# Kernel tuning notes

Hardware: AMD Instinct MI355X
Metric: run time of the kernel (lower is better)

The kernel has to match this reference:

```python
import jax, jax.numpy as jnp
import numpy as np

N_ENT = 50000
N_REL = 200
N_EDGE = 1_000_000
D = 64


def setup_inputs() -> dict:
    key = jax.random.key(0)
    ks = jax.random.split(key, 12)
    src = jax.random.randint(ks[0], (N_EDGE,), 0, N_ENT)
    rel = jax.random.randint(ks[1], (N_EDGE,), 0, N_REL)
    dst = jax.random.randint(ks[2], (N_EDGE,), 0, N_ENT)
    triples = jnp.stack([src, rel, dst], axis=1).astype(jnp.int64)  # [E,3]
    s = 1.0 / np.sqrt(D)
    return {
        "emb_e": jax.random.normal(ks[3], (N_ENT, D), jnp.float32) * s,
        "re_att": jax.random.normal(ks[4], (N_REL,), jnp.float32) * 0.1,
        "W1": jax.random.normal(ks[5], (D, D), jnp.float32) * s,
        "W2": jax.random.normal(ks[6], (D, D), jnp.float32) * s,
        "W3": jax.random.normal(ks[7], (D, D), jnp.float32) * s,
        "u": jax.random.normal(ks[8], (3 * D,), jnp.float32) * s,
        "en_weight": jax.random.normal(ks[9], (D, D), jnp.float32) * s,
        "re_weight": jax.random.normal(ks[10], (D, D), jnp.float32) * s,
        "re_spec": jax.random.normal(ks[11], (D,), jnp.float32) * s,
        "triples": triples,
    }


def _forward(emb_e, re_att, W1, W2, W3, u, en_weight, re_weight, re_spec, triples):
    src = triples[:, 0]
    rel = triples[:, 1]
    dst = triples[:, 2]
    n = emb_e.shape[0]

    def wgc(x, W):
        # relation-weighted message passing: out[s] += w[r] * x[d]
        msg = jax.ops.segment_sum(x[dst] * re_att[rel][:, None], src, num_segments=n)
        return jnp.tanh((x + msg) @ W)

    x = wgc(emb_e, W1)
    x = wgc(x, W2)
    x = wgc(x, W3)

    # GAT-style edge scores: e = LeakyReLU(u . [W_en h_i ; W_re r_spec ; W_en h_j])
    d = x.shape[1]
    hs = x @ en_weight.T                       # [N,d] = (en_weight @ h)^T rows
    z_src = hs @ u[:d]                         # [N]
    z_dst = hs @ u[2 * d:]                     # [N]
    z_mid = u[d:2 * d] @ (re_weight @ re_spec)  # scalar, same for every edge
    scores = jax.nn.leaky_relu(z_src[src] + z_mid + z_dst[dst], 0.01)  # [E]

    # softmax normalized over ALL triples (global denominator, per source code)
    alpha = jax.nn.softmax(scores)

    # out[src] += alpha_e * x[dst]
    out = jax.ops.segment_sum(alpha[:, None] * x[dst], src, num_segments=n)
    return out


def reference(emb_e, re_att, W1, W2, W3, u, en_weight, re_weight, re_spec, triples):
    return _forward(emb_e, re_att, W1, W2, W3, u, en_weight, re_weight, re_spec, triples)
```

## Files before the change

### kernel.cpp

```cpp
#include <hip/hip_runtime.h>
#include <math.h>

#define N_ENT  50000
#define N_REL  200
#define N_EDGE 1000000
#define CHUNK  196
#define ECH    7813
#define NRNG   6250

#define WS_MISC   0
#define WS_ZSUM   128
#define WS_ZMID   192
#define WS_AV     256
#define WS_BV     512
#define WS_BSUM   0x000E0000
#define WS_BBASE  0x000F0000
#define WS_CNT8   0x00100000
#define WS_RBASE  0x00300000
#define WS_TOT    0x00500000
#define WS_OFFS   0x00540000
#define WS_ZSRC   0x00580000
#define WS_ZDST   0x005C0000
#define WS_SNODE  0x00600000
#define WS_EPK    0x00640000
#define WS_EA     0x00A40000
#define WS_EB     0x00E40000
#define WS_XB1    0x00A40000
#define WS_XB0    0x01240000

__device__ __forceinline__ float bflo(unsigned u) { return __uint_as_float(u << 16); }
__device__ __forceinline__ float bfhi(unsigned u) { return __uint_as_float(u & 0xffff0000u); }
__device__ __forceinline__ unsigned short f2bf(float f) {
  unsigned u = __float_as_uint(f);
  unsigned r = ((u >> 16) & 1u) + 0x7fffu;
  return (unsigned short)((u + r) >> 16);
}
__device__ __forceinline__ float lanebc(float v, int k) {
  return __uint_as_float((unsigned)__builtin_amdgcn_readlane((int)__float_as_uint(v), k));
}
__device__ __forceinline__ float fast_tanh(float x) {
  float ex = __expf(2.f * x);
  return 1.f - __fdividef(2.f, ex + 1.f);
}
__device__ __forceinline__ void fma8(float* acc, float wt, uint4 q) {
  acc[0] += wt * bflo(q.x); acc[1] += wt * bfhi(q.x);
  acc[2] += wt * bflo(q.y); acc[3] += wt * bfhi(q.y);
  acc[4] += wt * bflo(q.z); acc[5] += wt * bfhi(q.z);
  acc[6] += wt * bflo(q.w); acc[7] += wt * bfhi(q.w);
}

__global__ void k_init(const void* tri, int* cnt8, int* misc, double* zsum) {
  int i = blockIdx.x * blockDim.x + threadIdx.x;
  if (i < 8 * N_ENT) cnt8[i] = 0;
  if (blockIdx.x == 0 && threadIdx.x < 64) {
    int l = threadIdx.x;
    int z = ((const int*)tri)[2 * l + 1];
    unsigned long long m = __ballot(z == 0);
    if (l == 0) { misc[0] = (m == ~0ull) ? 1 : 0; *zsum = 0.0; }
  }
}

__global__ void k_conv(const float* __restrict__ x, unsigned short* __restrict__ xb) {
  int i = blockIdx.x * blockDim.x + threadIdx.x;
  if (i >= N_ENT * 16) return;
  float4 v = ((const float4*)x)[i];
  ushort4 o;
  o.x = f2bf(v.x); o.y = f2bf(v.y); o.z = f2bf(v.z); o.w = f2bf(v.w);
  ((ushort4*)xb)[i] = o;
}

__global__ void k_decode(const void* tri, int* __restrict__ cnt8,
                         unsigned* __restrict__ ea, unsigned* __restrict__ eb,
                         const int* misc) {
  int is64 = misc[0];
  int rep = blockIdx.x & 7;
  int stride = gridDim.x * blockDim.x;
  if (is64) {
    const long long* t = (const long long*)tri;
    for (int e = blockIdx.x * blockDim.x + threadIdx.x; e < N_EDGE; e += stride) {
      int s = (int)t[3 * e], r = (int)t[3 * e + 1], d = (int)t[3 * e + 2];
      int rk = atomicAdd(&cnt8[rep * N_ENT + s], 1);
      ea[e] = ((unsigned)s << 16) | ((unsigned)rep << 13) | (unsigned)rk;
      eb[e] = ((unsigned)r << 16) | (unsigned)d;
    }
  } else {
    const int* t = (const int*)tri;
    for (int e = blockIdx.x * blockDim.x + threadIdx.x; e < N_EDGE; e += stride) {
      int s = t[3 * e], r = t[3 * e + 1], d = t[3 * e + 2];
      int rk = atomicAdd(&cnt8[rep * N_ENT + s], 1);
      ea[e] = ((unsigned)s << 16) | ((unsigned)rep << 13) | (unsigned)rk;
      eb[e] = ((unsigned)r << 16) | (unsigned)d;
    }
  }
}

__global__ void k_merge(const int* __restrict__ cnt8, int* __restrict__ rbase,
                        int* __restrict__ tot) {
  int s = blockIdx.x * blockDim.x + threadIdx.x;
  if (s >= N_ENT) return;
  int run = 0;
#pragma unroll
  for (int rep = 0; rep < 8; rep++) {
    rbase[rep * N_ENT + s] = run;
    run += cnt8[rep * N_ENT + s];
  }
  tot[s] = run;
}

__global__ void k_scanA(const int* __restrict__ counts, int* __restrict__ bsum) {
  __shared__ int sm[4];
  int t = threadIdx.x;
  int i = blockIdx.x * CHUNK + t;
  int v = (t < CHUNK && i < N_ENT) ? counts[i] : 0;
  for (int o = 32; o; o >>= 1) v += __shfl_down(v, o);
  if ((t & 63) == 0) sm[t >> 6] = v;
  __syncthreads();
  if (t == 0) bsum[blockIdx.x] = sm[0] + sm[1] + sm[2] + sm[3];
}

__global__ void k_scanB(const int* __restrict__ bsum, int* __restrict__ bbase, int* __restrict__ offs) {
  __shared__ int sm[256];
  int t = threadIdx.x;
  int v = bsum[t];
  sm[t] = v;
  __syncthreads();
  for (int d = 1; d < 256; d <<= 1) {
    int x = (t >= d) ? sm[t - d] : 0;
    __syncthreads();
    sm[t] += x;
    __syncthreads();
  }
  bbase[t] = sm[t] - v;
  if (t == 255) offs[N_ENT] = sm[255];
}

__global__ void k_scanC(const int* __restrict__ counts, const int* __restrict__ bbase,
                        int* __restrict__ offs) {
  __shared__ int sm[256];
  int t = threadIdx.x;
  int i = blockIdx.x * CHUNK + t;
  int v = (t < CHUNK && i < N_ENT) ? counts[i] : 0;
  sm[t] = v;
  __syncthreads();
  for (int d = 1; d < 256; d <<= 1) {
    int x = (t >= d) ? sm[t - d] : 0;
    __syncthreads();
    sm[t] += x;
    __syncthreads();
  }
  if (t < CHUNK && i < N_ENT)
    offs[i] = bbase[blockIdx.x] + sm[t] - v;
}

__global__ void k_scatter(const unsigned* __restrict__ ea, const unsigned* __restrict__ eb,
                          const int* __restrict__ offs, const int* __restrict__ rbase,
                          unsigned* __restrict__ epk) {
  int q = blockIdx.x >> 3, x = blockIdx.x & 7;
  int lo = q * ECH, hi = lo + ECH;
  if (hi > N_EDGE) hi = N_EDGE;
  for (int e = lo + threadIdx.x; e < hi; e += 256) {
    unsigned a = ea[e];
    int s = a >> 16;
    if (s / NRNG == x) {
      int rep = (a >> 13) & 7;
      int rk = a & 8191;
      epk[offs[s] + rbase[rep * N_ENT + s] + rk] = eb[e];
    }
  }
}

__global__ void k_pre(const float* u, const float* enw, const float* rew, const float* rsp,
                      float* a, float* b, float* zmid) {
  int k = threadIdx.x;
  float aa = 0.f, bb = 0.f;
  for (int j = 0; j < 64; j++) {
    float w = enw[j * 64 + k];
    aa += u[j] * w;
    bb += u[128 + j] * w;
  }
  a[k] = aa; b[k] = bb;
  float t = 0.f;
  for (int c = 0; c < 64; c++) t += rew[k * 64 + c] * rsp[c];
  t *= u[64 + k];
  for (int o = 32; o; o >>= 1) t += __shfl_down(t, o);
  if (k == 0) *zmid = t;
}

template <int EPI>
__global__ void __launch_bounds__(256) k_wgc(
    const unsigned short* __restrict__ xb, const float* __restrict__ W,
    const int* __restrict__ offs, const unsigned* __restrict__ epk,
    const float* __restrict__ re_att, unsigned short* __restrict__ yb,
    const float* __restrict__ a, const float* __restrict__ b,
    float* __restrict__ zsrc, float* __restrict__ zdst) {
  __shared__ float s_att[N_REL];
  for (int t = threadIdx.x; t < N_REL; t += 256) s_att[t] = re_att[t];
  __syncthreads();
  int wid = (blockIdx.x * blockDim.x + threadIdx.x) >> 6;
  int lane = threadIdx.x & 63;
  if (wid >= N_ENT) return;
  int node = wid;
  int g = lane >> 3, c8 = (lane & 7) * 8;
  int e0 = offs[node], e1 = offs[node + 1];
  float acc[8] = {0.f, 0.f, 0.f, 0.f, 0.f, 0.f, 0.f, 0.f};
  {
    uint4 q = *(const uint4*)(xb + (size_t)node * 64 + c8);
    fma8(acc, (g == 0) ? 1.f : 0.f, q);
  }
  for (int e = e0; e < e1; e += 16) {
    int ia = e + g, ib = ia + 8;
    bool va = ia < e1, vb = ib < e1;
    unsigned pa = epk[va ? ia : e0];
    unsigned pb = epk[vb ? ib : e0];
    float wa = va ? s_att[pa >> 16] : 0.f;
    float wb = vb ? s_att[pb >> 16] : 0.f;
    uint4 qa = *(const uint4*)(xb + (size_t)(pa & 0xffffu) * 64 + c8);
    uint4 qb = *(const uint4*)(xb + (size_t)(pb & 0xffffu) * 64 + c8);
    fma8(acc, wa, qa);
    fma8(acc, wb, qb);
  }
#pragma unroll
  for (int off = 8; off <= 32; off <<= 1)
#pragma unroll
    for (int c = 0; c < 8; c++) acc[c] += __shfl_xor(acc[c], off);
  float o = 0.f;
#pragma unroll
  for (int j = 0; j < 8; j++)
#pragma unroll
    for (int c = 0; c < 8; c++)
      o += lanebc(acc[c], j) * W[(j * 8 + c) * 64 + lane];
  float yv = fast_tanh(o);
  yb[(size_t)node * 64 + lane] = f2bf(yv);
  if (EPI) {
    float za = yv * a[lane], zb = yv * b[lane];
    for (int s = 32; s; s >>= 1) { za += __shfl_down(za, s); zb += __shfl_down(zb, s); }
    if (lane == 0) { zsrc[node] = za; zdst[node] = zb; }
  }
}

__global__ void __launch_bounds__(256) k_out(
    const unsigned short* __restrict__ xb, const int* __restrict__ offs,
    const unsigned* __restrict__ epk, const float* __restrict__ zs,
    const float* __restrict__ zd, const float* zmid,
    float* __restrict__ out, float* __restrict__ snode) {
  int wid = (blockIdx.x * blockDim.x + threadIdx.x) >> 6;
  int lane = threadIdx.x & 63;
  if (wid >= N_ENT) return;
  int node = wid;
  int g = lane >> 3, c8 = (lane & 7) * 8;
  float zi = zs[node] + *zmid;
  float acc[8] = {0.f, 0.f, 0.f, 0.f, 0.f, 0.f, 0.f, 0.f};
  float s0 = 0.f;
  int e0 = offs[node], e1 = offs[node + 1];
  for (int e = e0; e < e1; e += 16) {
    int ia = e + g, ib = ia + 8;
    bool va = ia < e1, vb = ib < e1;
    unsigned pa = epk[va ? ia : e0];
    unsigned pb = epk[vb ? ib : e0];
    int da = pa & 0xffffu, db = pb & 0xffffu;
    float ca = zi + zd[da];
    float cb = zi + zd[db];
    ca = ca >= 0.f ? ca : 0.01f * ca;
    cb = cb >= 0.f ? cb : 0.01f * cb;
    float wa = va ? __expf(ca) : 0.f;
    float wb = vb ? __expf(cb) : 0.f;
    uint4 qa = *(const uint4*)(xb + (size_t)da * 64 + c8);
    uint4 qb = *(const uint4*)(xb + (size_t)db * 64 + c8);
    fma8(acc, wa, qa);
    fma8(acc, wb, qb);
    s0 += wa + wb;
  }
#pragma unroll
  for (int off = 8; off <= 32; off <<= 1) {
#pragma unroll
    for (int c = 0; c < 8; c++) acc[c] += __shfl_xor(acc[c], off);
    s0 += __shfl_xor(s0, off);
  }
  if (lane < 8) {
    float4* p = (float4*)(out + (size_t)node * 64 + lane * 8);
    p[0] = make_float4(acc[0], acc[1], acc[2], acc[3]);
    p[1] = make_float4(acc[4], acc[5], acc[6], acc[7]);
  }
  if (lane == 0) snode[node] = s0;
}

__global__ void k_red(const float* __restrict__ snode, double* zsum) {
  int stride = gridDim.x * blockDim.x;
  double s = 0.0;
  for (int i = blockIdx.x * blockDim.x + threadIdx.x; i < N_ENT; i += stride)
    s += (double)snode[i];
  for (int o = 32; o; o >>= 1) s += __shfl_down(s, o);
  __shared__ double ws_[4];
  if ((threadIdx.x & 63) == 0) ws_[threadIdx.x >> 6] = s;
  __syncthreads();
  if (threadIdx.x == 0)
    atomicAdd(zsum, ws_[0] + ws_[1] + ws_[2] + ws_[3]);
}

__global__ void k_norm(float* __restrict__ out, const double* zsum) {
  int i = blockIdx.x * blockDim.x + threadIdx.x;
  if (i >= N_ENT * 16) return;
  float invZ = (float)(1.0 / *zsum);
  float4 v = ((float4*)out)[i];
  v.x *= invZ; v.y *= invZ; v.z *= invZ; v.w *= invZ;
  ((float4*)out)[i] = v;
}

extern "C" void kernel_launch(void* const* d_in, const int* in_sizes, int n_in,
                              void* d_out, int out_size, void* d_ws, size_t ws_size,
                              hipStream_t stream) {
  const float* emb   = (const float*)d_in[0];
  const float* reatt = (const float*)d_in[1];
  const float* W1    = (const float*)d_in[2];
  const float* W2    = (const float*)d_in[3];
  const float* W3    = (const float*)d_in[4];
  const float* u     = (const float*)d_in[5];
  const float* enw   = (const float*)d_in[6];
  const float* rew   = (const float*)d_in[7];
  const float* rsp   = (const float*)d_in[8];
  const void*  tri   = d_in[9];

  char* ws = (char*)d_ws;
  int*            misc   = (int*)(ws + WS_MISC);
  double*         zsum   = (double*)(ws + WS_ZSUM);
  float*          zmid   = (float*)(ws + WS_ZMID);
  float*          av     = (float*)(ws + WS_AV);
  float*          bv     = (float*)(ws + WS_BV);
  int*            bsum   = (int*)(ws + WS_BSUM);
  int*            bbase  = (int*)(ws + WS_BBASE);
  int*            cnt8   = (int*)(ws + WS_CNT8);
  int*            rbase  = (int*)(ws + WS_RBASE);
  int*            tot    = (int*)(ws + WS_TOT);
  int*            offs   = (int*)(ws + WS_OFFS);
  float*          zsrc   = (float*)(ws + WS_ZSRC);
  float*          zdst   = (float*)(ws + WS_ZDST);
  float*          snode  = (float*)(ws + WS_SNODE);
  unsigned*       epk    = (unsigned*)(ws + WS_EPK);
  unsigned*       ea     = (unsigned*)(ws + WS_EA);
  unsigned*       eb     = (unsigned*)(ws + WS_EB);
  unsigned short* xb0    = (unsigned short*)(ws + WS_XB0);
  unsigned short* xb1    = (unsigned short*)(ws + WS_XB1);
  float*          out    = (float*)d_out;

  k_init<<<1563, 256, 0, stream>>>(tri, cnt8, misc, zsum);
  k_conv<<<3125, 256, 0, stream>>>(emb, xb0);
  k_decode<<<4096, 256, 0, stream>>>(tri, cnt8, ea, eb, misc);
  k_merge<<<196, 256, 0, stream>>>(cnt8, rbase, tot);
  k_scanA<<<256, 256, 0, stream>>>(tot, bsum);
  k_scanB<<<1, 256, 0, stream>>>(bsum, bbase, offs);
  k_scanC<<<256, 256, 0, stream>>>(tot, bbase, offs);
  k_scatter<<<1024, 256, 0, stream>>>(ea, eb, offs, rbase, epk);
  k_pre<<<1, 64, 0, stream>>>(u, enw, rew, rsp, av, bv, zmid);

  int nb = (N_ENT * 64 + 255) / 256;
  k_wgc<0><<<nb, 256, 0, stream>>>(xb0, W1, offs, epk, reatt, xb1, nullptr, nullptr, nullptr, nullptr);
  k_wgc<0><<<nb, 256, 0, stream>>>(xb1, W2, offs, epk, reatt, xb0, nullptr, nullptr, nullptr, nullptr);
  k_wgc<1><<<nb, 256, 0, stream>>>(xb0, W3, offs, epk, reatt, xb1, av, bv, zsrc, zdst);

  k_out<<<nb, 256, 0, stream>>>(xb1, offs, epk, zsrc, zdst, zmid, out, snode);
  k_red<<<196, 256, 0, stream>>>(snode, zsum);
  k_norm<<<3125, 256, 0, stream>>>(out, zsum);
}
```

Measured before the change: 243.8 us.

## Replace global-atomic CSR build with shared-memory chunked histogram and scatter

Edge bucketing by source no longer uses global atomics into 8 replicated count arrays. It now builds per-chunk histograms in LDS for each of 8 node ranges, scans them per node across 64 chunks to get chunk bases, and scatters using LDS atomics for local ranks. This removes contended global atomics and the large count-array zeroing, at the cost of an extra pass over the source ids and a serial 64-step scan per node. The gather loops also clamp invalid lanes to row 0 instead of reading a stale index.

```diff
diff --git a/kernel.cpp b/kernel.cpp
--- a/kernel.cpp
+++ b/kernel.cpp
@@ -5,7 +5,9 @@
 #define N_REL  200
 #define N_EDGE 1000000
 #define CHUNK  196
-#define ECH    7813
+#define NCH    64
+#define ECH2   15625
+#define NPART  8
 #define NRNG   6250
 
 #define WS_MISC   0
@@ -13,20 +15,19 @@
 #define WS_ZMID   192
 #define WS_AV     256
 #define WS_BV     512
-#define WS_BSUM   0x000E0000
-#define WS_BBASE  0x000F0000
-#define WS_CNT8   0x00100000
-#define WS_RBASE  0x00300000
-#define WS_TOT    0x00500000
-#define WS_OFFS   0x00540000
-#define WS_ZSRC   0x00580000
-#define WS_ZDST   0x005C0000
-#define WS_SNODE  0x00600000
-#define WS_EPK    0x00640000
-#define WS_EA     0x00A40000
-#define WS_EB     0x00E40000
-#define WS_XB1    0x00A40000
-#define WS_XB0    0x01240000
+#define WS_BSUM   0x00010000
+#define WS_BBASE  0x00011000
+#define WS_TOT    0x00040000
+#define WS_OFFS   0x00080000
+#define WS_ZSRC   0x000C0000
+#define WS_ZDST   0x00100000
+#define WS_SNODE  0x00140000
+#define WS_SRCS   0x00180000
+#define WS_EB     0x00380000
+#define WS_EPK    0x00780000
+#define WS_HIST   0x00B80000
+#define WS_XB1    0x00B80000
+#define WS_XB0    0x01200000
 
 __device__ __forceinline__ float bflo(unsigned u) { return __uint_as_float(u << 16); }
 __device__ __forceinline__ float bfhi(unsigned u) { return __uint_as_float(u & 0xffff0000u); }
@@ -49,9 +50,7 @@
   acc[6] += wt * bflo(q.w); acc[7] += wt * bfhi(q.w);
 }
 
-__global__ void k_init(const void* tri, int* cnt8, int* misc, double* zsum) {
-  int i = blockIdx.x * blockDim.x + threadIdx.x;
-  if (i < 8 * N_ENT) cnt8[i] = 0;
+__global__ void k_init(const void* tri, int* misc, double* zsum) {
   if (blockIdx.x == 0 && threadIdx.x < 64) {
     int l = threadIdx.x;
     int z = ((const int*)tri)[2 * l + 1];
@@ -69,40 +68,52 @@
   ((ushort4*)xb)[i] = o;
 }
 
-__global__ void k_decode(const void* tri, int* __restrict__ cnt8,
-                         unsigned* __restrict__ ea, unsigned* __restrict__ eb,
-                         const int* misc) {
+__global__ void k_decode(const void* tri, unsigned short* __restrict__ srcs,
+                         unsigned* __restrict__ eb, const int* misc) {
   int is64 = misc[0];
-  int rep = blockIdx.x & 7;
   int stride = gridDim.x * blockDim.x;
   if (is64) {
     const long long* t = (const long long*)tri;
     for (int e = blockIdx.x * blockDim.x + threadIdx.x; e < N_EDGE; e += stride) {
       int s = (int)t[3 * e], r = (int)t[3 * e + 1], d = (int)t[3 * e + 2];
-      int rk = atomicAdd(&cnt8[rep * N_ENT + s], 1);
-      ea[e] = ((unsigned)s << 16) | ((unsigned)rep << 13) | (unsigned)rk;
+      srcs[e] = (unsigned short)s;
       eb[e] = ((unsigned)r << 16) | (unsigned)d;
     }
   } else {
     const int* t = (const int*)tri;
     for (int e = blockIdx.x * blockDim.x + threadIdx.x; e < N_EDGE; e += stride) {
       int s = t[3 * e], r = t[3 * e + 1], d = t[3 * e + 2];
-      int rk = atomicAdd(&cnt8[rep * N_ENT + s], 1);
-      ea[e] = ((unsigned)s << 16) | ((unsigned)rep << 13) | (unsigned)rk;
+      srcs[e] = (unsigned short)s;
       eb[e] = ((unsigned)r << 16) | (unsigned)d;
     }
   }
 }
 
-__global__ void k_merge(const int* __restrict__ cnt8, int* __restrict__ rbase,
-                        int* __restrict__ tot) {
+__global__ void __launch_bounds__(256) k_hist(const unsigned short* __restrict__ srcs,
+                                              unsigned short* __restrict__ hist) {
+  __shared__ unsigned h[NRNG];
+  int c = blockIdx.x >> 3, x = blockIdx.x & 7;
+  int lo = x * NRNG;
+  for (int i = threadIdx.x; i < NRNG; i += 256) h[i] = 0u;
+  __syncthreads();
+  int e0 = c * ECH2, e1 = e0 + ECH2;
+  for (int e = e0 + threadIdx.x; e < e1; e += 256) {
+    int rel = (int)srcs[e] - lo;
+    if ((unsigned)rel < NRNG) atomicAdd(&h[rel], 1u);
+  }
+  __syncthreads();
+  for (int i = threadIdx.x; i < NRNG; i += 256)
+    hist[c * N_ENT + lo + i] = (unsigned short)h[i];
+}
+
+__global__ void k_scanH(unsigned short* __restrict__ hist, int* __restrict__ tot) {
   int s = blockIdx.x * blockDim.x + threadIdx.x;
   if (s >= N_ENT) return;
   int run = 0;
-#pragma unroll
-  for (int rep = 0; rep < 8; rep++) {
-    rbase[rep * N_ENT + s] = run;
-    run += cnt8[rep * N_ENT + s];
+  for (int c = 0; c < NCH; c++) {
+    int v = hist[c * N_ENT + s];
+    hist[c * N_ENT + s] = (unsigned short)run;
+    run += v;
   }
   tot[s] = run;
 }
@@ -152,19 +163,22 @@
     offs[i] = bbase[blockIdx.x] + sm[t] - v;
 }
 
-__global__ void k_scatter(const unsigned* __restrict__ ea, const unsigned* __restrict__ eb,
-                          const int* __restrict__ offs, const int* __restrict__ rbase,
-                          unsigned* __restrict__ epk) {
-  int q = blockIdx.x >> 3, x = blockIdx.x & 7;
-  int lo = q * ECH, hi = lo + ECH;
-  if (hi > N_EDGE) hi = N_EDGE;
-  for (int e = lo + threadIdx.x; e < hi; e += 256) {
-    unsigned a = ea[e];
-    int s = a >> 16;
-    if (s / NRNG == x) {
-      int rep = (a >> 13) & 7;
-      int rk = a & 8191;
-      epk[offs[s] + rbase[rep * N_ENT + s] + rk] = eb[e];
+__global__ void __launch_bounds__(256) k_scatter(
+    const unsigned short* __restrict__ srcs, const unsigned* __restrict__ eb,
+    const unsigned short* __restrict__ cbase, const int* __restrict__ offs,
+    unsigned* __restrict__ epk) {
+  __shared__ unsigned h[NRNG];
+  int c = blockIdx.x >> 3, x = blockIdx.x & 7;
+  int lo = x * NRNG;
+  for (int i = threadIdx.x; i < NRNG; i += 256) h[i] = 0u;
+  __syncthreads();
+  int e0 = c * ECH2, e1 = e0 + ECH2;
+  for (int e = e0 + threadIdx.x; e < e1; e += 256) {
+    int s = (int)srcs[e];
+    int rel = s - lo;
+    if ((unsigned)rel < NRNG) {
+      int lr = atomicAdd(&h[rel], 1u);
+      epk[offs[s] + (int)cbase[c * N_ENT + s] + lr] = eb[e];
     }
   }
 }
@@ -214,8 +228,10 @@
     unsigned pb = epk[vb ? ib : e0];
     float wa = va ? s_att[pa >> 16] : 0.f;
     float wb = vb ? s_att[pb >> 16] : 0.f;
-    uint4 qa = *(const uint4*)(xb + (size_t)(pa & 0xffffu) * 64 + c8);
-    uint4 qb = *(const uint4*)(xb + (size_t)(pb & 0xffffu) * 64 + c8);
+    unsigned ra = va ? (pa & 0xffffu) : 0u;
+    unsigned rb = vb ? (pb & 0xffffu) : 0u;
+    uint4 qa = *(const uint4*)(xb + (size_t)ra * 64 + c8);
+    uint4 qb = *(const uint4*)(xb + (size_t)rb * 64 + c8);
     fma8(acc, wa, qa);
     fma8(acc, wb, qb);
   }
@@ -257,7 +273,8 @@
     bool va = ia < e1, vb = ib < e1;
     unsigned pa = epk[va ? ia : e0];
     unsigned pb = epk[vb ? ib : e0];
-    int da = pa & 0xffffu, db = pb & 0xffffu;
+    unsigned da = va ? (pa & 0xffffu) : 0u;
+    unsigned db = vb ? (pb & 0xffffu) : 0u;
     float ca = zi + zd[da];
     float cb = zi + zd[db];
     ca = ca >= 0.f ? ca : 0.01f * ca;
@@ -328,28 +345,28 @@
   float*          bv     = (float*)(ws + WS_BV);
   int*            bsum   = (int*)(ws + WS_BSUM);
   int*            bbase  = (int*)(ws + WS_BBASE);
-  int*            cnt8   = (int*)(ws + WS_CNT8);
-  int*            rbase  = (int*)(ws + WS_RBASE);
   int*            tot    = (int*)(ws + WS_TOT);
   int*            offs   = (int*)(ws + WS_OFFS);
   float*          zsrc   = (float*)(ws + WS_ZSRC);
   float*          zdst   = (float*)(ws + WS_ZDST);
   float*          snode  = (float*)(ws + WS_SNODE);
+  unsigned short* srcs   = (unsigned short*)(ws + WS_SRCS);
+  unsigned*       eb     = (unsigned*)(ws + WS_EB);
   unsigned*       epk    = (unsigned*)(ws + WS_EPK);
-  unsigned*       ea     = (unsigned*)(ws + WS_EA);
-  unsigned*       eb     = (unsigned*)(ws + WS_EB);
+  unsigned short* hist   = (unsigned short*)(ws + WS_HIST);
   unsigned short* xb0    = (unsigned short*)(ws + WS_XB0);
   unsigned short* xb1    = (unsigned short*)(ws + WS_XB1);
   float*          out    = (float*)d_out;
 
-  k_init<<<1563, 256, 0, stream>>>(tri, cnt8, misc, zsum);
+  k_init<<<1, 64, 0, stream>>>(tri, misc, zsum);
   k_conv<<<3125, 256, 0, stream>>>(emb, xb0);
-  k_decode<<<4096, 256, 0, stream>>>(tri, cnt8, ea, eb, misc);
-  k_merge<<<196, 256, 0, stream>>>(cnt8, rbase, tot);
+  k_decode<<<4096, 256, 0, stream>>>(tri, srcs, eb, misc);
+  k_hist<<<NCH * NPART, 256, 0, stream>>>(srcs, hist);
+  k_scanH<<<196, 256, 0, stream>>>(hist, tot);
   k_scanA<<<256, 256, 0, stream>>>(tot, bsum);
   k_scanB<<<1, 256, 0, stream>>>(bsum, bbase, offs);
   k_scanC<<<256, 256, 0, stream>>>(tot, bbase, offs);
-  k_scatter<<<1024, 256, 0, stream>>>(ea, eb, offs, rbase, epk);
+  k_scatter<<<NCH * NPART, 256, 0, stream>>>(srcs, eb, hist, offs, epk);
   k_pre<<<1, 64, 0, stream>>>(u, enw, rew, rsp, av, bv, zmid);
 
   int nb = (N_ENT * 64 + 255) / 256;
```

New measurement: 250.1 us. 2.6% more time.
